# Kernel tuning notes

Measured on AMD Instinct MI355X. Metric: run time of the kernel, lower is better.

## Reference

```python
import jax, jax.numpy as jnp
import numpy as np

S = 64    # shapelets_size
N = 256   # num_shapelets
C = 3     # in_channels
B = 64
L = 2048


def setup_inputs() -> dict:
    key = jax.random.key(0)
    kx, ks = jax.random.split(key)
    x = jax.random.normal(kx, (B, C, L), dtype=jnp.float32)
    shapelets = jax.random.normal(ks, (C, N, S), dtype=jnp.float32)
    return {"x": x, "shapelets": shapelets}


def reference(x, shapelets):
    # x: (B, C, L); shapelets: (C, N, S)
    W = x.shape[2] - S + 1  # number of sliding windows
    # unfold: (B, C, W, S)
    idx = jnp.arange(W)[:, None] + jnp.arange(S)[None, :]
    win = x[:, :, idx]
    # cdist with mm-based euclidean: d^2 = |a|^2 + |b|^2 - 2 a.b
    win_sq = jnp.sum(win * win, axis=-1)                 # (B, C, W)
    shp_sq = jnp.sum(shapelets * shapelets, axis=-1)     # (C, N)
    cross = jnp.einsum('bcws,cns->bcwn', win, shapelets)  # (B, C, W, N)
    d2 = win_sq[..., None] + shp_sq[None, :, None, :] - 2.0 * cross
    d = jnp.sqrt(jnp.maximum(d2, 0.0))                   # (B, C, W, N)
    # sum over channels, keepdim -> (B, 1, W, N); transpose -> (B, 1, N, W); min over W
    summed = jnp.sum(d, axis=1, keepdims=True)
    out = jnp.min(jnp.swapaxes(summed, 2, 3), axis=3)    # (B, 1, N)
    return out
```

## Files before the change

kernel.cpp:

```cpp
#include <hip/hip_runtime.h>


typedef float  v4f __attribute__((ext_vector_type(4)));
typedef short  v8s __attribute__((ext_vector_type(8)));
typedef unsigned short u16;
typedef unsigned int   u32;
typedef unsigned long long u64;

#define S_ 64
#define N_ 256
#define C_ 3
#define B_ 64
#define L_ 2048
#define W_ 1985
#define WQL 512
#define NC 146
#define CSTRIDE 146
#define THREADS 512

__device__ __forceinline__ u16 f2bf(float f) {
    u32 u = __builtin_bit_cast(u32, f);
    return (u16)((u + 0x7FFFu + ((u >> 16) & 1u)) >> 16);
}
__device__ __forceinline__ float bf2f(u16 b) {
    return __builtin_bit_cast(float, ((u32)b) << 16);
}

__global__ __launch_bounds__(THREADS, 4)
void shapelet_min_kernel(const float* __restrict__ x,
                         const float* __restrict__ shp,
                         float* __restrict__ out)
{
    __shared__ u64   xls[C_ * 8 * CSTRIDE];
    __shared__ float wsq[C_][WQL];
    __shared__ u16   scratch[C_ * 64 * 72];
    __shared__ float red[8][64];

    const int tid  = threadIdx.x;
    const int wave = tid >> 6;
    const int lane = tid & 63;
    const int m    = lane & 15;
    const int q    = lane >> 4;
    const int ww   = wave & 3;
    const int wn   = wave >> 2;
    const int blk  = blockIdx.x;
    const int wq   = blk & 3;
    const int nh   = (blk >> 2) & 1;
    const int b    = blk >> 3;
    const int w0   = wq << 9;
    const int wlen = min(WQL, W_ - w0);

    const float* xb = x + (size_t)b * (C_ * L_);
    float xf[8];
    int xc = 0, xt = 0;
    bool xact = (tid < C_ * NC);
    if (xact) {
        xc = tid / NC;
        xt = tid - xc * NC;
        int e = w0 + (xt << 2);
        if (e + 7 < L_) {
            v4f a0 = *(const v4f*)(xb + xc * L_ + e);
            v4f a1 = *(const v4f*)(xb + xc * L_ + e + 4);
            xf[0] = a0[0]; xf[1] = a0[1]; xf[2] = a0[2]; xf[3] = a0[3];
            xf[4] = a1[0]; xf[5] = a1[1]; xf[6] = a1[2]; xf[7] = a1[3];
        } else {
            #pragma unroll
            for (int i = 0; i < 8; ++i)
                xf[i] = (e + i < L_) ? xb[xc * L_ + e + i] : 0.f;
        }
    }

    const int nbase = nh << 7;
    #pragma unroll
    for (int k = 0; k < 6; ++k) {
        int idx = tid + k * THREADS;
        int sq = idx & 15;
        int n  = (idx >> 4) & 63;
        int c  = idx >> 10;
        v4f v = *(const v4f*)(shp + ((size_t)(c * N_ + nbase + n) * S_ + (sq << 2)));
        u64 pk = (u64)f2bf(v[0]) | ((u64)f2bf(v[1]) << 16)
               | ((u64)f2bf(v[2]) << 32) | ((u64)f2bf(v[3]) << 48);
        *(u64*)(scratch + ((c * 64 + n) * 72 + (sq << 2))) = pk;
    }

    if (xact) {
        u16 w8[8];
        #pragma unroll
        for (int i = 0; i < 8; ++i) w8[i] = f2bf(-2.f * xf[i]);
        #pragma unroll
        for (int r = 0; r < 4; ++r) {
            u64 pk = (u64)w8[r] | ((u64)w8[r + 1] << 16)
                   | ((u64)w8[r + 2] << 32) | ((u64)w8[r + 3] << 48);
            xls[(xc * 8 + r) * CSTRIDE + xt] = pk;
            if (xt > 0) xls[(xc * 8 + r + 4) * CSTRIDE + xt - 1] = pk;
        }
    }
    __syncthreads();

    if (tid < 128 * C_) {
        int c  = tid >> 7;
        int t0 = tid & 127;
        const u64* cp0 = &xls[(c * 8) * CSTRIDE];
        u64 ch = cp0[t0];
        float h0 = bf2f((u16)ch),         h1 = bf2f((u16)(ch >> 16)),
              h2 = bf2f((u16)(ch >> 32)), h3 = bf2f((u16)(ch >> 48));
        float sq0 = h0 * h0, sq1 = h1 * h1, sq2 = h2 * h2;
        float s = sq0 + sq1 + sq2 + h3 * h3;
        #pragma unroll
        for (int kk = 1; kk < 16; ++kk) {
            u64 c2 = cp0[t0 + kk];
            float e0 = bf2f((u16)c2),         e1 = bf2f((u16)(c2 >> 16)),
                  e2 = bf2f((u16)(c2 >> 32)), e3 = bf2f((u16)(c2 >> 48));
            s += e0 * e0; s += e1 * e1; s += e2 * e2; s += e3 * e3;
        }
        u64 ct = cp0[t0 + 16];
        float t4 = bf2f((u16)ct), t5 = bf2f((u16)(ct >> 16)), t6 = bf2f((u16)(ct >> 32));
        float s0 = s;
        float s1 = s0 - sq0 + t4 * t4;
        float s2 = s1 - sq1 + t5 * t5;
        float s3 = s2 - sq2 + t6 * t6;
        v4f o = (v4f){0.25f * s0, 0.25f * s1, 0.25f * s2, 0.25f * s3};
        *(v4f*)&wsq[c][t0 << 2] = o;
    }

    const int rp = m & 7;
    const int mE = m >> 3;

    #pragma unroll 1
    for (int g = 0; g < 2; ++g) {
        v8s bfr[C_][2][2];
        float ssq[C_][2];
        #pragma unroll
        for (int c = 0; c < C_; ++c) {
            #pragma unroll
            for (int nt = 0; nt < 2; ++nt) {
                float sacc = 0.f;
                #pragma unroll
                for (int h = 0; h < 2; ++h) {
                    v8s f = *(const v8s*)(scratch +
                             ((c * 64 + wn * 32 + nt * 16 + m) * 72 + h * 32 + q * 8));
                    bfr[c][nt][h] = f;
                    #pragma unroll
                    for (int j = 0; j < 8; ++j) {
                        float e = bf2f((u16)f[j]);
                        sacc += e * e;
                    }
                }
                sacc += __shfl_xor(sacc, 16);
                sacc += __shfl_xor(sacc, 32);
                ssq[c][nt] = sacc;
            }
        }
        __syncthreads();

        float minv[2] = {1e30f, 1e30f};
        #pragma unroll 1
        for (int it = 0; it < 8; ++it) {
            const int wb = it * 64 + ww * 16;
            if (wb >= wlen) continue;

            const int bidx = (wb >> 2) + 2 * mE + 2 * q;
            v8s afr[C_][2];
            #pragma unroll
            for (int c = 0; c < C_; ++c) {
                const u64* cp = &xls[(c * 8 + rp) * CSTRIDE];
                afr[c][0] = *(const v8s*)(cp + bidx);
                afr[c][1] = *(const v8s*)(cp + bidx + 8);
            }

            v4f acc[C_][2];
            #pragma unroll
            for (int c = 0; c < C_; ++c) {
                v4f wv = *(const v4f*)&wsq[c][wb + (q << 2)];
                #pragma unroll
                for (int nt = 0; nt < 2; ++nt)
                    #pragma unroll
                    for (int gi = 0; gi < 4; ++gi)
                        acc[c][nt][gi] = wv[gi] + ssq[c][nt];
            }

            __builtin_amdgcn_s_setprio(1);
            #pragma unroll
            for (int c = 0; c < C_; ++c)
                #pragma unroll
                for (int nt = 0; nt < 2; ++nt) {
                    acc[c][nt] = __builtin_amdgcn_mfma_f32_16x16x32_bf16(
                        afr[c][0], bfr[c][nt][0], acc[c][nt], 0, 0, 0);
                    acc[c][nt] = __builtin_amdgcn_mfma_f32_16x16x32_bf16(
                        afr[c][1], bfr[c][nt][1], acc[c][nt], 0, 0, 0);
                }
            __builtin_amdgcn_s_setprio(0);

            if (wb + 16 <= wlen) {
                #pragma unroll
                for (int nt = 0; nt < 2; ++nt)
                    #pragma unroll
                    for (int gi = 0; gi < 4; ++gi) {
                        float t = __builtin_amdgcn_sqrtf(fmaxf(acc[0][nt][gi], 0.f))
                                + __builtin_amdgcn_sqrtf(fmaxf(acc[1][nt][gi], 0.f))
                                + __builtin_amdgcn_sqrtf(fmaxf(acc[2][nt][gi], 0.f));
                        minv[nt] = fminf(minv[nt], t);
                    }
            } else {
                #pragma unroll
                for (int nt = 0; nt < 2; ++nt)
                    #pragma unroll
                    for (int gi = 0; gi < 4; ++gi) {
                        float t = __builtin_amdgcn_sqrtf(fmaxf(acc[0][nt][gi], 0.f))
                                + __builtin_amdgcn_sqrtf(fmaxf(acc[1][nt][gi], 0.f))
                                + __builtin_amdgcn_sqrtf(fmaxf(acc[2][nt][gi], 0.f));
                        bool ok = (wb + (q << 2) + gi) < wlen;
                        minv[nt] = fminf(minv[nt], ok ? t : 1e30f);
                    }
            }
        }

        #pragma unroll
        for (int nt = 0; nt < 2; ++nt) {
            minv[nt] = fminf(minv[nt], __shfl_xor(minv[nt], 16));
            minv[nt] = fminf(minv[nt], __shfl_xor(minv[nt], 32));
        }

        if (g == 0) {
            #pragma unroll
            for (int k = 0; k < 6; ++k) {
                int idx = tid + k * THREADS;
                int sq = idx & 15;
                int n  = (idx >> 4) & 63;
                int c  = idx >> 10;
                v4f v = *(const v4f*)(shp +
                        ((size_t)(c * N_ + nbase + 64 + n) * S_ + (sq << 2)));
                u64 pk = (u64)f2bf(v[0]) | ((u64)f2bf(v[1]) << 16)
                       | ((u64)f2bf(v[2]) << 32) | ((u64)f2bf(v[3]) << 48);
                *(u64*)(scratch + ((c * 64 + n) * 72 + (sq << 2))) = pk;
            }
        }
        if (lane < 16) {
            red[wave][wn * 32 + lane]      = minv[0];
            red[wave][wn * 32 + 16 + lane] = minv[1];
        }
        __syncthreads();

        if (tid < 64) {
            int tn = tid >> 5;
            float v = red[tn * 4 + 0][tid];
            v = fminf(v, red[tn * 4 + 1][tid]);
            v = fminf(v, red[tn * 4 + 2][tid]);
            v = fminf(v, red[tn * 4 + 3][tid]);
            atomicMin((u32*)out + ((size_t)b * N_ + nbase + (g << 6) + tid),
                      __float_as_uint(v));
        }
        if (g == 0) __syncthreads();
    }
}

extern "C" void kernel_launch(void* const* d_in, const int* in_sizes, int n_in,
                              void* d_out, int out_size, void* d_ws, size_t ws_size,
                              hipStream_t stream) {
    const float* x   = (const float*)d_in[0];
    const float* shp = (const float*)d_in[1];
    hipMemsetAsync(d_out, 0x7f, (size_t)B_ * N_ * sizeof(float), stream);
    hipLaunchKernelGGL(shapelet_min_kernel, dim3(512), dim3(THREADS), 0, stream,
                       x, shp, (float*)d_out);
}
```

Before: 91.80 us.

## Fold norm terms into an extra MFMA and shrink shifted x layout

The window and shapelet squared norms are now added inside the matrix core. An extra 16x16x32 bf16 MFMA multiplies a hi/lo bf16-split norm vector by a ones vector, replacing the per-element VALU adds that initialised the accumulators. The shifted-window LDS layout also drops from 8 to 4 copies per channel, using offset row indexing and 64-bit reads instead of 128-bit ones. This removes VALU work and LDS footprint but adds one MFMA per tile (three instead of two) and more, narrower LDS loads. It also drops the s_setprio hints.

```diff
diff --git a/kernel.cpp b/kernel.cpp
--- a/kernel.cpp
+++ b/kernel.cpp
@@ -2,6 +2,7 @@
 
 
 typedef float  v4f __attribute__((ext_vector_type(4)));
+typedef unsigned int v4u __attribute__((ext_vector_type(4)));
 typedef short  v8s __attribute__((ext_vector_type(8)));
 typedef unsigned short u16;
 typedef unsigned int   u32;
@@ -15,7 +16,7 @@
 #define W_ 1985
 #define WQL 512
 #define NC 146
-#define CSTRIDE 146
+#define CSTRIDE 160
 #define THREADS 512
 
 __device__ __forceinline__ u16 f2bf(float f) {
@@ -24,6 +25,12 @@
 }
 __device__ __forceinline__ float bf2f(u16 b) {
     return __builtin_bit_cast(float, ((u32)b) << 16);
+}
+__device__ __forceinline__ u32 pack2bf(float v) {
+    u16 hi = f2bf(v);
+    float r = v - bf2f(hi);
+    u16 lo = f2bf(r);
+    return (u32)hi | ((u32)lo << 16);
 }
 
 __global__ __launch_bounds__(THREADS, 4)
@@ -31,9 +38,9 @@
                          const float* __restrict__ shp,
                          float* __restrict__ out)
 {
-    __shared__ u64   xls[C_ * 8 * CSTRIDE];
-    __shared__ float wsq[C_][WQL];
-    __shared__ u16   scratch[C_ * 64 * 72];
+    __shared__ u64 xls[C_ * 4 * CSTRIDE];
+    __shared__ u32 wnt[C_][WQL];
+    __shared__ u16 scratch[C_ * 64 * 72];
     __shared__ float red[8][64];
 
     const int tid  = threadIdx.x;
@@ -49,6 +56,9 @@
     const int b    = blk >> 3;
     const int w0   = wq << 9;
     const int wlen = min(WQL, W_ - w0);
+
+    const u32 c11 = (q == 0) ? 0x3F803F80u : 0u;
+    const v4f kz  = (v4f){0.f, 0.f, 0.f, 0.f};
 
     const float* xb = x + (size_t)b * (C_ * L_);
     float xf[8];
@@ -91,8 +101,7 @@
         for (int r = 0; r < 4; ++r) {
             u64 pk = (u64)w8[r] | ((u64)w8[r + 1] << 16)
                    | ((u64)w8[r + 2] << 32) | ((u64)w8[r + 3] << 48);
-            xls[(xc * 8 + r) * CSTRIDE + xt] = pk;
-            if (xt > 0) xls[(xc * 8 + r + 4) * CSTRIDE + xt - 1] = pk;
+            xls[(xc * 4 + r) * CSTRIDE + 4 * r + xt] = pk;
         }
     }
     __syncthreads();
@@ -100,7 +109,7 @@
     if (tid < 128 * C_) {
         int c  = tid >> 7;
         int t0 = tid & 127;
-        const u64* cp0 = &xls[(c * 8) * CSTRIDE];
+        const u64* cp0 = &xls[(c * 4) * CSTRIDE];
         u64 ch = cp0[t0];
         float h0 = bf2f((u16)ch),         h1 = bf2f((u16)(ch >> 16)),
               h2 = bf2f((u16)(ch >> 32)), h3 = bf2f((u16)(ch >> 48));
@@ -119,17 +128,19 @@
         float s1 = s0 - sq0 + t4 * t4;
         float s2 = s1 - sq1 + t5 * t5;
         float s3 = s2 - sq2 + t6 * t6;
-        v4f o = (v4f){0.25f * s0, 0.25f * s1, 0.25f * s2, 0.25f * s3};
-        *(v4f*)&wsq[c][t0 << 2] = o;
-    }
-
-    const int rp = m & 7;
-    const int mE = m >> 3;
+        v4u o = (v4u){pack2bf(0.25f * s0), pack2bf(0.25f * s1),
+                      pack2bf(0.25f * s2), pack2bf(0.25f * s3)};
+        *(v4u*)&wnt[c][t0 << 2] = o;
+    }
+
+    const int r  = m & 3;
+    const int sE = m >> 2;
+    union U8 { u32 w[4]; v8s v; };
 
     #pragma unroll 1
     for (int g = 0; g < 2; ++g) {
         v8s bfr[C_][2][2];
-        float ssq[C_][2];
+        v8s bnorm[C_][2];
         #pragma unroll
         for (int c = 0; c < C_; ++c) {
             #pragma unroll
@@ -148,7 +159,11 @@
                 }
                 sacc += __shfl_xor(sacc, 16);
                 sacc += __shfl_xor(sacc, 32);
-                ssq[c][nt] = sacc;
+                U8 bn;
+                bn.w[0] = c11;
+                bn.w[1] = (q == 0) ? pack2bf(sacc) : 0u;
+                bn.w[2] = 0u; bn.w[3] = 0u;
+                bnorm[c][nt] = bn.v;
             }
         }
         __syncthreads();
@@ -159,37 +174,32 @@
             const int wb = it * 64 + ww * 16;
             if (wb >= wlen) continue;
 
-            const int bidx = (wb >> 2) + 2 * mE + 2 * q;
-            v8s afr[C_][2];
+            v4f acc[C_][2];
             #pragma unroll
             for (int c = 0; c < C_; ++c) {
-                const u64* cp = &xls[(c * 8 + rp) * CSTRIDE];
-                afr[c][0] = *(const v8s*)(cp + bidx);
-                afr[c][1] = *(const v8s*)(cp + bidx + 8);
-            }
-
-            v4f acc[C_][2];
-            #pragma unroll
-            for (int c = 0; c < C_; ++c) {
-                v4f wv = *(const v4f*)&wsq[c][wb + (q << 2)];
-                #pragma unroll
-                for (int nt = 0; nt < 2; ++nt)
-                    #pragma unroll
-                    for (int gi = 0; gi < 4; ++gi)
-                        acc[c][nt][gi] = wv[gi] + ssq[c][nt];
-            }
-
-            __builtin_amdgcn_s_setprio(1);
-            #pragma unroll
-            for (int c = 0; c < C_; ++c)
+                const u64* cp = &xls[(c * 4 + r) * CSTRIDE + 4 * r];
+                const int T0 = (wb >> 2) + 2 * q + sE;
+                union { u64 u[2]; v8s v; } a0, a1;
+                a0.u[0] = cp[T0];     a0.u[1] = cp[T0 + 1];
+                a1.u[0] = cp[T0 + 8]; a1.u[1] = cp[T0 + 9];
+
+                u32 nv = wnt[c][wb + m];
+                U8 an;
+                an.w[0] = (q == 0) ? nv : 0u;
+                an.w[1] = c11;
+                an.w[2] = 0u; an.w[3] = 0u;
+
                 #pragma unroll
                 for (int nt = 0; nt < 2; ++nt) {
-                    acc[c][nt] = __builtin_amdgcn_mfma_f32_16x16x32_bf16(
-                        afr[c][0], bfr[c][nt][0], acc[c][nt], 0, 0, 0);
-                    acc[c][nt] = __builtin_amdgcn_mfma_f32_16x16x32_bf16(
-                        afr[c][1], bfr[c][nt][1], acc[c][nt], 0, 0, 0);
+                    v4f a = __builtin_amdgcn_mfma_f32_16x16x32_bf16(
+                                an.v, bnorm[c][nt], kz, 0, 0, 0);
+                    a = __builtin_amdgcn_mfma_f32_16x16x32_bf16(
+                                a0.v, bfr[c][nt][0], a, 0, 0, 0);
+                    a = __builtin_amdgcn_mfma_f32_16x16x32_bf16(
+                                a1.v, bfr[c][nt][1], a, 0, 0, 0);
+                    acc[c][nt] = a;
                 }
-            __builtin_amdgcn_s_setprio(0);
+            }
 
             if (wb + 16 <= wlen) {
                 #pragma unroll
```

New measurement: 87.01 us. 1.05x faster.

## Skew the bf16 window layout and prefetch next-iteration MFMA A fragments

Applied to the files above, without the earlier changes.

The shared bf16 window buffer shrinks from 8 shifted copies per channel to 4 rows. Each row is offset by 4*r with a padded stride, and the duplicate shifted store is gone. The A-operand fragments are now gathered as two 64-bit loads each and double-buffered, so the next iteration's LDS reads are issued before the current MFMAs and epilogue. The setprio hints are removed, and the early skip for out-of-range window tiles is dropped, so those tiles are computed and masked. This targets LDS read latency and bank conflicts at the cost of more registers and some wasted masked work on the tail block.

```diff
diff --git a/kernel.cpp b/kernel.cpp
--- a/kernel.cpp
+++ b/kernel.cpp
@@ -15,7 +15,7 @@
 #define W_ 1985
 #define WQL 512
 #define NC 146
-#define CSTRIDE 146
+#define CSTRIDE 160
 #define THREADS 512
 
 __device__ __forceinline__ u16 f2bf(float f) {
@@ -31,7 +31,7 @@
                          const float* __restrict__ shp,
                          float* __restrict__ out)
 {
-    __shared__ u64   xls[C_ * 8 * CSTRIDE];
+    __shared__ u64   xls[C_ * 4 * CSTRIDE];
     __shared__ float wsq[C_][WQL];
     __shared__ u16   scratch[C_ * 64 * 72];
     __shared__ float red[8][64];
@@ -91,8 +91,7 @@
         for (int r = 0; r < 4; ++r) {
             u64 pk = (u64)w8[r] | ((u64)w8[r + 1] << 16)
                    | ((u64)w8[r + 2] << 32) | ((u64)w8[r + 3] << 48);
-            xls[(xc * 8 + r) * CSTRIDE + xt] = pk;
-            if (xt > 0) xls[(xc * 8 + r + 4) * CSTRIDE + xt - 1] = pk;
+            xls[(xc * 4 + r) * CSTRIDE + 4 * r + xt] = pk;
         }
     }
     __syncthreads();
@@ -100,7 +99,7 @@
     if (tid < 128 * C_) {
         int c  = tid >> 7;
         int t0 = tid & 127;
-        const u64* cp0 = &xls[(c * 8) * CSTRIDE];
+        const u64* cp0 = &xls[(c * 4) * CSTRIDE];
         u64 ch = cp0[t0];
         float h0 = bf2f((u16)ch),         h1 = bf2f((u16)(ch >> 16)),
               h2 = bf2f((u16)(ch >> 32)), h3 = bf2f((u16)(ch >> 48));
@@ -123,8 +122,9 @@
         *(v4f*)&wsq[c][t0 << 2] = o;
     }
 
-    const int rp = m & 7;
-    const int mE = m >> 3;
+    const int r  = m & 3;
+    const int sE = m >> 2;
+    const int Tq = 2 * q + sE;
 
     #pragma unroll 1
     for (int g = 0; g < 2; ++g) {
@@ -153,19 +153,36 @@
         }
         __syncthreads();
 
+        v8s afc[C_][2];
+        {
+            const int T0 = ((ww * 16) >> 2) + Tq;
+            #pragma unroll
+            for (int c = 0; c < C_; ++c) {
+                const u64* cp = &xls[(c * 4 + r) * CSTRIDE + 4 * r];
+                union { u64 u[2]; v8s v; } a0, a1;
+                a0.u[0] = cp[T0];     a0.u[1] = cp[T0 + 1];
+                a1.u[0] = cp[T0 + 8]; a1.u[1] = cp[T0 + 9];
+                afc[c][0] = a0.v; afc[c][1] = a1.v;
+            }
+        }
+
         float minv[2] = {1e30f, 1e30f};
         #pragma unroll 1
         for (int it = 0; it < 8; ++it) {
-            const int wb = it * 64 + ww * 16;
-            if (wb >= wlen) continue;
-
-            const int bidx = (wb >> 2) + 2 * mE + 2 * q;
-            v8s afr[C_][2];
-            #pragma unroll
-            for (int c = 0; c < C_; ++c) {
-                const u64* cp = &xls[(c * 8 + rp) * CSTRIDE];
-                afr[c][0] = *(const v8s*)(cp + bidx);
-                afr[c][1] = *(const v8s*)(cp + bidx + 8);
+            const int wb  = it * 64 + ww * 16;
+            const int wbn = (it < 7) ? wb + 64 : ww * 16;
+
+            v8s afn[C_][2];
+            {
+                const int Tn = (wbn >> 2) + Tq;
+                #pragma unroll
+                for (int c = 0; c < C_; ++c) {
+                    const u64* cp = &xls[(c * 4 + r) * CSTRIDE + 4 * r];
+                    union { u64 u[2]; v8s v; } a0, a1;
+                    a0.u[0] = cp[Tn];     a0.u[1] = cp[Tn + 1];
+                    a1.u[0] = cp[Tn + 8]; a1.u[1] = cp[Tn + 9];
+                    afn[c][0] = a0.v; afn[c][1] = a1.v;
+                }
             }
 
             v4f acc[C_][2];
@@ -178,18 +195,15 @@
                     for (int gi = 0; gi < 4; ++gi)
                         acc[c][nt][gi] = wv[gi] + ssq[c][nt];
             }
-
-            __builtin_amdgcn_s_setprio(1);
             #pragma unroll
             for (int c = 0; c < C_; ++c)
                 #pragma unroll
                 for (int nt = 0; nt < 2; ++nt) {
                     acc[c][nt] = __builtin_amdgcn_mfma_f32_16x16x32_bf16(
-                        afr[c][0], bfr[c][nt][0], acc[c][nt], 0, 0, 0);
+                        afc[c][0], bfr[c][nt][0], acc[c][nt], 0, 0, 0);
                     acc[c][nt] = __builtin_amdgcn_mfma_f32_16x16x32_bf16(
-                        afr[c][1], bfr[c][nt][1], acc[c][nt], 0, 0, 0);
+                        afc[c][1], bfr[c][nt][1], acc[c][nt], 0, 0, 0);
                 }
-            __builtin_amdgcn_s_setprio(0);
 
             if (wb + 16 <= wlen) {
                 #pragma unroll
@@ -212,6 +226,12 @@
                         bool ok = (wb + (q << 2) + gi) < wlen;
                         minv[nt] = fminf(minv[nt], ok ? t : 1e30f);
                     }
+            }
+
+            #pragma unroll
+            for (int c = 0; c < C_; ++c) {
+                afc[c][0] = afn[c][0];
+                afc[c][1] = afn[c][1];
             }
         }
 
```

Result: no change. 92.11 us (+0.3%).
